# Performance work log

Hardware: AMD Instinct MI355X
Metric: run time of the kernel (lower is better)

Reference implementation:

```python
import jax, jax.numpy as jnp
import numpy as np

# Constraint of the (buggy) original module: batch N == num_heads H == embed_size E, head_dim = 1,
# and value_len == key_len == query_len == L.
E = 64   # embed_size == num_heads == batch
H = 64
N = 64
L = 256
LN_EPS = 1e-5


def setup_inputs() -> dict:
    key = jax.random.key(0)
    ks = jax.random.split(key, 4)
    return {
        "values": jax.random.normal(ks[0], (N, L, E), dtype=jnp.float32),
        "keys": jax.random.normal(ks[1], (N, L, E), dtype=jnp.float32),
        "query": jax.random.normal(ks[2], (N, L, E), dtype=jnp.float32),
        # fc_out params (torch nn.Linear: y = x @ W.T + b)
        "W_out": jax.random.normal(ks[3], (E, E), dtype=jnp.float32) / np.float32(np.sqrt(E)),
        "b_out": jnp.zeros((E,), dtype=jnp.float32),
        # LayerNorm params
        "ln_w": jnp.ones((E,), dtype=jnp.float32),
        "ln_b": jnp.zeros((E,), dtype=jnp.float32),
    }


def reference(values, keys, query, W_out, b_out, ln_w, ln_b):
    Nb, Lq, Emb = query.shape
    Hh = H
    hd = Emb // Hh  # == 1

    def split_heads(x):
        # [N, L, E] -> [N, L, H, hd] -> permute(2,0,1,3) -> [H, N, L, hd]
        return x.reshape(Nb, -1, Hh, hd).transpose(2, 0, 1, 3)

    v = split_heads(values)   # [H, N, Lv, hd]
    k = split_heads(keys)     # [H, N, Lk, hd]
    q = split_heads(query)    # [H, N, Lq, hd]

    # torch.einsum('qnhd,knhd->qnk') on [H,N,L,hd] tensors: contract over (seq, head_dim)
    energy = jnp.einsum('anld,bnld->anb', q, k)            # [H, N, H]
    attn = jax.nn.softmax(energy / jnp.sqrt(jnp.float32(hd)), axis=-1)

    # torch.einsum('qnk,nkhd->qnhd') with values [H,N,Lv,hd]; requires N == H
    out = jnp.einsum('qnk,nkld->qnld', attn, v)            # [H, N, Lv, hd]

    # permute(1,2,0,3) -> [N, Lv, H, hd] -> view(N, Lq, E)
    out = out.transpose(1, 2, 0, 3).reshape(Nb, Lq, Emb)
    out = out @ W_out.T + b_out                            # fc_out, [N, Lq, E]

    # residual against the PERMUTED query [H,N,L,1] broadcasts to [H, N, Lq, E]
    x = out + q

    mu = jnp.mean(x, axis=-1, keepdims=True)
    var = jnp.var(x, axis=-1, keepdims=True)
    return (x - mu) / jnp.sqrt(var + LN_EPS) * ln_w + ln_b
```

## Files before the change

kernel.cpp:

```cpp
#include <hip/hip_runtime.h>
#include <stdint.h>

#define L_SEQ 256
#define E_DIM 64
#define N_B   64
#define LN_EPS 1e-5f

typedef float f4 __attribute__((ext_vector_type(4)));

__global__ __launch_bounds__(256) void attn_softmax_kernel(
    const float* __restrict__ gq,
    const float* __restrict__ gk,
    float* __restrict__ ws)
{
    __shared__ float Qs[L_SEQ * E_DIM];
    __shared__ float Ks[L_SEQ * E_DIM];

    const int t = threadIdx.x;
    const int n = blockIdx.x;
    const float* qb = gq + (size_t)n * (L_SEQ * E_DIM);
    const float* kb = gk + (size_t)n * (L_SEQ * E_DIM);

    #pragma unroll
    for (int i = 0; i < 16; ++i) {
        reinterpret_cast<f4*>(Qs)[t + 256 * i] =
            reinterpret_cast<const f4*>(qb)[t + 256 * i];
        reinterpret_cast<f4*>(Ks)[t + 256 * i] =
            reinterpret_cast<const f4*>(kb)[t + 256 * i];
    }
    __syncthreads();

    const int tx = t & 15, ty = t >> 4;
    const int b0 = tx * 4, a0 = ty * 4;

    float acc[4][4] = {};
    #pragma unroll 8
    for (int l = 0; l < L_SEQ; ++l) {
        f4 qa = *reinterpret_cast<const f4*>(&Qs[l * E_DIM + a0]);
        f4 kv = *reinterpret_cast<const f4*>(&Ks[l * E_DIM + b0]);
        #pragma unroll
        for (int ia = 0; ia < 4; ++ia)
            #pragma unroll
            for (int ib = 0; ib < 4; ++ib)
                acc[ia][ib] = fmaf(qa[ia], kv[ib], acc[ia][ib]);
    }

    #pragma unroll
    for (int ia = 0; ia < 4; ++ia) {
        float m = fmaxf(fmaxf(acc[ia][0], acc[ia][1]),
                        fmaxf(acc[ia][2], acc[ia][3]));
        #pragma unroll
        for (int s = 1; s <= 8; s <<= 1) m = fmaxf(m, __shfl_xor(m, s));
        float e0 = __expf(acc[ia][0] - m);
        float e1 = __expf(acc[ia][1] - m);
        float e2 = __expf(acc[ia][2] - m);
        float e3 = __expf(acc[ia][3] - m);
        float ssum = (e0 + e1) + (e2 + e3);
        #pragma unroll
        for (int s = 1; s <= 8; s <<= 1) ssum += __shfl_xor(ssum, s);
        float inv = 1.0f / ssum;
        acc[ia][0] = e0 * inv; acc[ia][1] = e1 * inv;
        acc[ia][2] = e2 * inv; acc[ia][3] = e3 * inv;
    }

    float* wbase = ws + n * 4096 + a0;
    #pragma unroll
    for (int ib = 0; ib < 4; ++ib) {
        f4 v4 = {acc[0][ib], acc[1][ib], acc[2][ib], acc[3][ib]};
        *reinterpret_cast<f4*>(wbase + (size_t)(b0 + ib) * 64) = v4;
    }
}

__global__ __launch_bounds__(256) void out_ln_kernel(
    const float* __restrict__ gv,
    const float* __restrict__ gw,
    const float* __restrict__ gbo,
    const float* __restrict__ glnw,
    const float* __restrict__ glnb,
    const float* __restrict__ ws,
    float*       __restrict__ gout)
{
    __shared__ float Vl[E_DIM * N_B];
    __shared__ float Wt[64 * 68];
    __shared__ float Tt[64 * 64];

    const int t = threadIdx.x;
    const int l = blockIdx.x;

    #pragma unroll
    for (int i = 0; i < 4; ++i) {
        int idx4 = t + 256 * i;
        int k = idx4 >> 4, c = (idx4 & 15) * 4;
        reinterpret_cast<f4*>(Vl)[idx4] =
            *reinterpret_cast<const f4*>(gv + (size_t)k * (L_SEQ * E_DIM)
                                            + (size_t)l * E_DIM + c);
    }
    #pragma unroll
    for (int i = 0; i < 16; ++i) {
        int idx = t + 256 * i;
        int e = idx >> 6, j = idx & 63;
        Wt[j * 68 + e] = gw[idx];
    }
    __syncthreads();

    const int tx = t & 15, tg = t >> 4;
    const int j0 = tx * 4;
    const int n0 = tg * 4;

    float T[4][4] = {};
    #pragma unroll 4
    for (int k = 0; k < 64; ++k) {
        f4 vk = *reinterpret_cast<const f4*>(&Vl[k * 64 + n0]);
        #pragma unroll
        for (int in = 0; in < 4; ++in) {
            f4 a4 = *reinterpret_cast<const f4*>(
                ws + (size_t)(n0 + in) * 4096 + k * 64 + j0);
            #pragma unroll
            for (int jj = 0; jj < 4; ++jj)
                T[in][jj] = fmaf(a4[jj], vk[in], T[in][jj]);
        }
    }
    #pragma unroll
    for (int in = 0; in < 4; ++in) {
        f4 w4 = {T[in][0], T[in][1], T[in][2], T[in][3]};
        *reinterpret_cast<f4*>(&Tt[(n0 + in) * 64 + j0]) = w4;
    }
    __syncthreads();

    const int e0 = tx * 4;
    float fc[4][4] = {};
    #pragma unroll 4
    for (int jj = 0; jj < 64; jj += 4) {
        f4 t4[4];
        #pragma unroll
        for (int in = 0; in < 4; ++in)
            t4[in] = *reinterpret_cast<const f4*>(&Tt[(n0 + in) * 64 + jj]);
        #pragma unroll
        for (int m = 0; m < 4; ++m) {
            f4 w4 = *reinterpret_cast<const f4*>(&Wt[(jj + m) * 68 + e0]);
            #pragma unroll
            for (int in = 0; in < 4; ++in)
                #pragma unroll
                for (int ie = 0; ie < 4; ++ie)
                    fc[in][ie] = fmaf(t4[in][m], w4[ie], fc[in][ie]);
        }
    }

    float be[4], lw[4], lb[4];
    #pragma unroll
    for (int ie = 0; ie < 4; ++ie) {
        be[ie] = gbo[e0 + ie];
        lw[ie] = glnw[e0 + ie];
        lb[ie] = glnb[e0 + ie];
    }

    f4 o4[4];
    #pragma unroll
    for (int in = 0; in < 4; ++in) {
        float v0 = fc[in][0] + be[0];
        float v1 = fc[in][1] + be[1];
        float v2 = fc[in][2] + be[2];
        float v3 = fc[in][3] + be[3];
        float s1 = (v0 + v1) + (v2 + v3);
        float s2 = (v0 * v0 + v1 * v1) + (v2 * v2 + v3 * v3);
        #pragma unroll
        for (int s = 1; s <= 8; s <<= 1) {
            s1 += __shfl_xor(s1, s);
            s2 += __shfl_xor(s2, s);
        }
        float mu  = s1 * (1.0f / 64.0f);
        float var = s2 * (1.0f / 64.0f) - mu * mu;
        float rs  = rsqrtf(var + LN_EPS);
        o4[in][0] = (v0 - mu) * rs * lw[0] + lb[0];
        o4[in][1] = (v1 - mu) * rs * lw[1] + lb[1];
        o4[in][2] = (v2 - mu) * rs * lw[2] + lb[2];
        o4[in][3] = (v3 - mu) * rs * lw[3] + lb[3];
    }

    const size_t hstride = (size_t)N_B * L_SEQ * E_DIM;
    float* ob0 = gout + (size_t)n0 * (L_SEQ * E_DIM) + (size_t)l * E_DIM + e0;
    #pragma unroll 8
    for (int h = 0; h < 64; ++h) {
        float* op = ob0 + (size_t)h * hstride;
        #pragma unroll
        for (int in = 0; in < 4; ++in)
            __builtin_nontemporal_store(
                o4[in], reinterpret_cast<f4*>(op + (size_t)in * (L_SEQ * E_DIM)));
    }
}

extern "C" void kernel_launch(void* const* d_in, const int* in_sizes, int n_in,
                              void* d_out, int out_size, void* d_ws, size_t ws_size,
                              hipStream_t stream)
{
    const float* gv  = (const float*)d_in[0];
    const float* gk  = (const float*)d_in[1];
    const float* gq  = (const float*)d_in[2];
    const float* gw  = (const float*)d_in[3];
    const float* gbo = (const float*)d_in[4];
    const float* glw = (const float*)d_in[5];
    const float* glb = (const float*)d_in[6];
    float* wsAttn = (float*)d_ws;
    float* out    = (float*)d_out;

    hipLaunchKernelGGL(attn_softmax_kernel, dim3(64), dim3(256), 0, stream,
                       gq, gk, wsAttn);
    hipLaunchKernelGGL(out_ln_kernel, dim3(256), dim3(256), 0, stream,
                       gv, gw, gbo, glw, glb, wsAttn, out);
}
```

Before: 306.0 us.

## Fold fc_out into attention weights, fuse row compute, separate broadcast kernel

The attention softmax, the attn·V product and the fc_out projection are merged into one per-batch kernel. The matmuls are reassociated so that attn is first multiplied by W_out (64x64x64), and the result is then applied to V for each sequence position. LayerNorm'd rows are written to workspace. A separate lightweight kernel reads each row once and broadcasts it to all 64 heads with nontemporal stores. This removes the global attn round-trip and gives the dominant output write a simple, highly parallel 1024-block kernel, at the cost of a strided gather of V per batch and an extra workspace write/read.

```diff
diff --git a/kernel.cpp b/kernel.cpp
--- a/kernel.cpp
+++ b/kernel.cpp
@@ -8,13 +8,23 @@
 
 typedef float f4 __attribute__((ext_vector_type(4)));
 
-__global__ __launch_bounds__(256) void attn_softmax_kernel(
+__global__ __launch_bounds__(256) void fused_row_kernel(
     const float* __restrict__ gq,
     const float* __restrict__ gk,
-    float* __restrict__ ws)
+    const float* __restrict__ gv,
+    const float* __restrict__ gw,
+    const float* __restrict__ gbo,
+    const float* __restrict__ glnw,
+    const float* __restrict__ glnb,
+    float*       __restrict__ ws)
 {
-    __shared__ float Qs[L_SEQ * E_DIM];
-    __shared__ float Ks[L_SEQ * E_DIM];
+    __shared__ float lds[32768];
+    float* Qs    = lds;
+    float* Ks    = lds + 16384;
+    float* VnS   = lds;
+    float* attnS = lds + 16384;
+    float* WtS   = lds + 20480;
+    float* PS    = lds + 24576;
 
     const int t = threadIdx.x;
     const int n = blockIdx.x;
@@ -51,116 +61,87 @@
                         fmaxf(acc[ia][2], acc[ia][3]));
         #pragma unroll
         for (int s = 1; s <= 8; s <<= 1) m = fmaxf(m, __shfl_xor(m, s));
-        float e0 = __expf(acc[ia][0] - m);
-        float e1 = __expf(acc[ia][1] - m);
-        float e2 = __expf(acc[ia][2] - m);
-        float e3 = __expf(acc[ia][3] - m);
-        float ssum = (e0 + e1) + (e2 + e3);
+        float e0v = __expf(acc[ia][0] - m);
+        float e1v = __expf(acc[ia][1] - m);
+        float e2v = __expf(acc[ia][2] - m);
+        float e3v = __expf(acc[ia][3] - m);
+        float ssum = (e0v + e1v) + (e2v + e3v);
         #pragma unroll
         for (int s = 1; s <= 8; s <<= 1) ssum += __shfl_xor(ssum, s);
         float inv = 1.0f / ssum;
-        acc[ia][0] = e0 * inv; acc[ia][1] = e1 * inv;
-        acc[ia][2] = e2 * inv; acc[ia][3] = e3 * inv;
-    }
-
-    float* wbase = ws + n * 4096 + a0;
-    #pragma unroll
-    for (int ib = 0; ib < 4; ++ib) {
-        f4 v4 = {acc[0][ib], acc[1][ib], acc[2][ib], acc[3][ib]};
-        *reinterpret_cast<f4*>(wbase + (size_t)(b0 + ib) * 64) = v4;
-    }
-}
-
-__global__ __launch_bounds__(256) void out_ln_kernel(
-    const float* __restrict__ gv,
-    const float* __restrict__ gw,
-    const float* __restrict__ gbo,
-    const float* __restrict__ glnw,
-    const float* __restrict__ glnb,
-    const float* __restrict__ ws,
-    float*       __restrict__ gout)
-{
-    __shared__ float Vl[E_DIM * N_B];
-    __shared__ float Wt[64 * 68];
-    __shared__ float Tt[64 * 64];
-
-    const int t = threadIdx.x;
-    const int l = blockIdx.x;
-
-    #pragma unroll
-    for (int i = 0; i < 4; ++i) {
-        int idx4 = t + 256 * i;
-        int k = idx4 >> 4, c = (idx4 & 15) * 4;
-        reinterpret_cast<f4*>(Vl)[idx4] =
-            *reinterpret_cast<const f4*>(gv + (size_t)k * (L_SEQ * E_DIM)
-                                            + (size_t)l * E_DIM + c);
-    }
+        acc[ia][0] = e0v * inv; acc[ia][1] = e1v * inv;
+        acc[ia][2] = e2v * inv; acc[ia][3] = e3v * inv;
+    }
+
+    __syncthreads();
+
+    #pragma unroll
+    for (int ia = 0; ia < 4; ++ia) {
+        f4 v4 = {acc[ia][0], acc[ia][1], acc[ia][2], acc[ia][3]};
+        *reinterpret_cast<f4*>(&attnS[(a0 + ia) * 64 + b0]) = v4;
+    }
+
     #pragma unroll
     for (int i = 0; i < 16; ++i) {
         int idx = t + 256 * i;
-        int e = idx >> 6, j = idx & 63;
-        Wt[j * 68 + e] = gw[idx];
-    }
-    __syncthreads();
-
-    const int tx = t & 15, tg = t >> 4;
-    const int j0 = tx * 4;
-    const int n0 = tg * 4;
-
-    float T[4][4] = {};
+        WtS[(idx & 63) * 64 + (idx >> 6)] = gw[idx];
+    }
+
+    #pragma unroll
+    for (int k = 0; k < 64; ++k)
+        VnS[k * 256 + t] = gv[((size_t)k * 256 + (size_t)t) * 64 + n];
+
+    __syncthreads();
+
+    const int k0 = ty * 4, e0 = tx * 4;
+    float pacc[4][4] = {};
+    #pragma unroll 8
+    for (int q = 0; q < 64; ++q) {
+        f4 av = *reinterpret_cast<const f4*>(&attnS[q * 64 + k0]);
+        f4 wv = *reinterpret_cast<const f4*>(&WtS[q * 64 + e0]);
+        #pragma unroll
+        for (int ik = 0; ik < 4; ++ik)
+            #pragma unroll
+            for (int ie = 0; ie < 4; ++ie)
+                pacc[ik][ie] = fmaf(av[ik], wv[ie], pacc[ik][ie]);
+    }
+    #pragma unroll
+    for (int ik = 0; ik < 4; ++ik) {
+        f4 v4 = {pacc[ik][0], pacc[ik][1], pacc[ik][2], pacc[ik][3]};
+        *reinterpret_cast<f4*>(&PS[(k0 + ik) * 64 + e0]) = v4;
+    }
+
+    f4 be = *reinterpret_cast<const f4*>(&gbo[e0]);
+    f4 lw = *reinterpret_cast<const f4*>(&glnw[e0]);
+    f4 lb = *reinterpret_cast<const f4*>(&glnb[e0]);
+
+    __syncthreads();
+
+    const int l0 = ty * 16;
+    float fcv[16][4] = {};
     #pragma unroll 4
     for (int k = 0; k < 64; ++k) {
-        f4 vk = *reinterpret_cast<const f4*>(&Vl[k * 64 + n0]);
-        #pragma unroll
-        for (int in = 0; in < 4; ++in) {
-            f4 a4 = *reinterpret_cast<const f4*>(
-                ws + (size_t)(n0 + in) * 4096 + k * 64 + j0);
+        f4 p4 = *reinterpret_cast<const f4*>(&PS[k * 64 + e0]);
+        f4 vv[4];
+        #pragma unroll
+        for (int g = 0; g < 4; ++g)
+            vv[g] = *reinterpret_cast<const f4*>(&VnS[k * 256 + l0 + 4 * g]);
+        #pragma unroll
+        for (int g = 0; g < 4; ++g)
             #pragma unroll
-            for (int jj = 0; jj < 4; ++jj)
-                T[in][jj] = fmaf(a4[jj], vk[in], T[in][jj]);
-        }
-    }
-    #pragma unroll
-    for (int in = 0; in < 4; ++in) {
-        f4 w4 = {T[in][0], T[in][1], T[in][2], T[in][3]};
-        *reinterpret_cast<f4*>(&Tt[(n0 + in) * 64 + j0]) = w4;
-    }
-    __syncthreads();
-
-    const int e0 = tx * 4;
-    float fc[4][4] = {};
-    #pragma unroll 4
-    for (int jj = 0; jj < 64; jj += 4) {
-        f4 t4[4];
-        #pragma unroll
-        for (int in = 0; in < 4; ++in)
-            t4[in] = *reinterpret_cast<const f4*>(&Tt[(n0 + in) * 64 + jj]);
-        #pragma unroll
-        for (int m = 0; m < 4; ++m) {
-            f4 w4 = *reinterpret_cast<const f4*>(&Wt[(jj + m) * 68 + e0]);
-            #pragma unroll
-            for (int in = 0; in < 4; ++in)
+            for (int j = 0; j < 4; ++j)
                 #pragma unroll
                 for (int ie = 0; ie < 4; ++ie)
-                    fc[in][ie] = fmaf(t4[in][m], w4[ie], fc[in][ie]);
-        }
-    }
-
-    float be[4], lw[4], lb[4];
-    #pragma unroll
-    for (int ie = 0; ie < 4; ++ie) {
-        be[ie] = gbo[e0 + ie];
-        lw[ie] = glnw[e0 + ie];
-        lb[ie] = glnb[e0 + ie];
-    }
-
-    f4 o4[4];
-    #pragma unroll
-    for (int in = 0; in < 4; ++in) {
-        float v0 = fc[in][0] + be[0];
-        float v1 = fc[in][1] + be[1];
-        float v2 = fc[in][2] + be[2];
-        float v3 = fc[in][3] + be[3];
+                    fcv[g * 4 + j][ie] = fmaf(vv[g][j], p4[ie], fcv[g * 4 + j][ie]);
+    }
+
+    float* wbase = ws + (size_t)n * 16384 + (size_t)l0 * 64 + e0;
+    #pragma unroll
+    for (int il = 0; il < 16; ++il) {
+        float v0 = fcv[il][0] + be[0];
+        float v1 = fcv[il][1] + be[1];
+        float v2 = fcv[il][2] + be[2];
+        float v3 = fcv[il][3] + be[3];
         float s1 = (v0 + v1) + (v2 + v3);
         float s2 = (v0 * v0 + v1 * v1) + (v2 * v2 + v3 * v3);
         #pragma unroll
@@ -171,21 +152,35 @@
         float mu  = s1 * (1.0f / 64.0f);
         float var = s2 * (1.0f / 64.0f) - mu * mu;
         float rs  = rsqrtf(var + LN_EPS);
-        o4[in][0] = (v0 - mu) * rs * lw[0] + lb[0];
-        o4[in][1] = (v1 - mu) * rs * lw[1] + lb[1];
-        o4[in][2] = (v2 - mu) * rs * lw[2] + lb[2];
-        o4[in][3] = (v3 - mu) * rs * lw[3] + lb[3];
-    }
-
-    const size_t hstride = (size_t)N_B * L_SEQ * E_DIM;
-    float* ob0 = gout + (size_t)n0 * (L_SEQ * E_DIM) + (size_t)l * E_DIM + e0;
-    #pragma unroll 8
+        f4 o;
+        o[0] = (v0 - mu) * rs * lw[0] + lb[0];
+        o[1] = (v1 - mu) * rs * lw[1] + lb[1];
+        o[2] = (v2 - mu) * rs * lw[2] + lb[2];
+        o[3] = (v3 - mu) * rs * lw[3] + lb[3];
+        *reinterpret_cast<f4*>(wbase + (size_t)il * 64) = o;
+    }
+}
+
+__global__ __launch_bounds__(256) void bcast_kernel(
+    const float* __restrict__ ws,
+    float*       __restrict__ gout)
+{
+    const int t  = threadIdx.x;
+    const int b  = blockIdx.x;
+    const int n  = b >> 4;
+    const int lc = b & 15;
+    const int r  = t >> 4;
+    const int c  = t & 15;
+
+    const size_t row = (size_t)n * 16384 + (size_t)(lc * 16 + r) * 64
+                     + (size_t)c * 4;
+    f4 v = *reinterpret_cast<const f4*>(ws + row);
+
+    float* op = gout + row;
+    #pragma unroll
     for (int h = 0; h < 64; ++h) {
-        float* op = ob0 + (size_t)h * hstride;
-        #pragma unroll
-        for (int in = 0; in < 4; ++in)
-            __builtin_nontemporal_store(
-                o4[in], reinterpret_cast<f4*>(op + (size_t)in * (L_SEQ * E_DIM)));
+        __builtin_nontemporal_store(v, reinterpret_cast<f4*>(op));
+        op += (size_t)N_B * L_SEQ * E_DIM;
     }
 }
 
@@ -200,11 +195,11 @@
     const float* gbo = (const float*)d_in[4];
     const float* glw = (const float*)d_in[5];
     const float* glb = (const float*)d_in[6];
-    float* wsAttn = (float*)d_ws;
-    float* out    = (float*)d_out;
-
-    hipLaunchKernelGGL(attn_softmax_kernel, dim3(64), dim3(256), 0, stream,
-                       gq, gk, wsAttn);
-    hipLaunchKernelGGL(out_ln_kernel, dim3(256), dim3(256), 0, stream,
-                       gv, gw, gbo, glw, glb, wsAttn, out);
+    float* wsRow = (float*)d_ws;
+    float* out   = (float*)d_out;
+
+    hipLaunchKernelGGL(fused_row_kernel, dim3(64), dim3(256), 0, stream,
+                       gq, gk, gv, gw, gbo, glw, glb, wsRow);
+    hipLaunchKernelGGL(bcast_kernel, dim3(1024), dim3(256), 0, stream,
+                       wsRow, out);
 }
```

New measurement: 329.7 us. 1.08x slower.
